# Kernel tuning notes

Measured on AMD Instinct MI355X. Metric: run time of the kernel, lower is better.

## Reference

```python
import math
import jax, jax.numpy as jnp
import numpy as np

N_HEADS = 8
FACTOR = 1.0


def setup_inputs() -> dict:
    key = jax.random.key(0)
    ks = jax.random.split(key, 5)
    B, L, D = 8, 4096, 512
    scale = 0.02
    def w(k):
        return jax.random.normal(k, (D, D), jnp.float32) * scale
    return {
        "hidden_states": jax.random.normal(ks[0], (B, L, D), jnp.float32),
        "Wq": w(ks[1]), "bq": jnp.zeros((D,), jnp.float32),
        "Wk": w(ks[2]), "bk": jnp.zeros((D,), jnp.float32),
        "Wv": w(ks[3]), "bv": jnp.zeros((D,), jnp.float32),
        "Wo": w(ks[4]), "bo": jnp.zeros((D,), jnp.float32),
    }


def reference(hidden_states, Wq, bq, Wk, bk, Wv, bv, Wo, bo):
    B, L, D = hidden_states.shape
    H = N_HEADS
    Hd = D // H

    def proj(W, b):
        y = hidden_states @ W.T + b                      # [B, L, D]
        return y.reshape(B, L, H, Hd).transpose(0, 2, 3, 1)  # [B, H, Hd, L]

    q = proj(Wq, bq)
    k = proj(Wk, bk)
    v = proj(Wv, bv)

    # period-based auto-correlation via FFT: corr(tau) = sum_t q(t) k(t - tau)
    qf = jnp.fft.rfft(q, axis=-1)
    kf = jnp.fft.rfft(k, axis=-1)
    corr = jnp.fft.irfft(qf * jnp.conj(kf), n=L, axis=-1)   # [B, H, Hd, L]

    # time-delay aggregation (eval branch): per-batch top-k delays
    mean_corr = corr.mean(axis=(1, 2))                      # [B, L]
    top_k = int(FACTOR * math.log(L))
    weights, delays = jax.lax.top_k(mean_corr, top_k)       # [B, k]
    weights = jax.nn.softmax(weights, axis=-1)

    # circular gather: pattern[b,h,d,i,l] = v[b,h,d,(l + delay[b,i]) % L]
    idx = (jnp.arange(L)[None, None, :] + delays[:, :, None]) % L  # [B, k, L]
    gathered = jax.vmap(lambda vb, ib: vb[:, :, ib])(v, idx)       # [B, H, Hd, k, L]
    agg = jnp.einsum("bhdkl,bk->bhdl", gathered, weights)          # [B, H, Hd, L]

    ctx = agg.transpose(0, 3, 1, 2).reshape(B, L, D)        # [B, L, D]
    return ctx @ Wo.T + bo
```

## Files before the change

### kernel.cpp

```cpp
#include <hip/hip_runtime.h>
#include <math.h>

#define NB 8
#define NL 4096
#define ND 512
#define NK 8

typedef unsigned short ushort_t;
typedef __bf16 bf16x8 __attribute__((ext_vector_type(8)));
typedef float f32x4 __attribute__((ext_vector_type(4)));

__device__ __forceinline__ unsigned short f2bf(float x) {
    unsigned u = __builtin_bit_cast(unsigned, x);
    u += 0x7fff + ((u >> 16) & 1);
    return (unsigned short)(u >> 16);
}
__device__ __forceinline__ float bf2f(unsigned short b) {
    unsigned u = ((unsigned)b) << 16;
    return __builtin_bit_cast(float, u);
}

__global__ void k_smallgemm(const float* __restrict__ A, const float* __restrict__ Bm,
                            float* __restrict__ C, int sa_k, int sa_i, int sb_k, int sb_j) {
    int i = blockIdx.y * 16 + threadIdx.y;
    int j = blockIdx.x * 16 + threadIdx.x;
    float acc = 0.f;
    for (int k = 0; k < ND; ++k)
        acc += A[k * sa_k + i * sa_i] * Bm[k * sb_k + j * sb_j];
    C[i * ND + j] = acc;
}

__global__ void k_biasprep(const float* __restrict__ Wo, const float* __restrict__ bv,
                           const float* __restrict__ bo, float* __restrict__ bp) {
    int i = blockIdx.x * blockDim.x + threadIdx.x;
    float acc = bo[i];
    for (int k = 0; k < ND; ++k) acc += Wo[i * ND + k] * bv[k];
    bp[i] = acc;
}

__global__ __launch_bounds__(256) void k_split(const float* __restrict__ src,
                                               ushort_t* __restrict__ dst) {
    int gid = blockIdx.x * 256 + threadIdx.x;
    int row = gid >> 7;
    int kc = (gid & 127) * 4;
    float4 v = *(const float4*)(src + (size_t)row * ND + kc);
    ushort4 hi, lo;
    hi.x = f2bf(v.x); lo.x = f2bf(v.x - bf2f(hi.x));
    hi.y = f2bf(v.y); lo.y = f2bf(v.y - bf2f(hi.y));
    hi.z = f2bf(v.z); lo.z = f2bf(v.z - bf2f(hi.z));
    hi.w = f2bf(v.w); lo.w = f2bf(v.w - bf2f(hi.w));
    *(ushort4*)(dst + (size_t)row * 1024 + kc) = hi;
    *(ushort4*)(dst + (size_t)row * 1024 + 512 + kc) = lo;
}

__global__ __launch_bounds__(256) void k_transpose(const float* __restrict__ X,
                                                   float* __restrict__ XT) {
    __shared__ float t[32][33];
    int b  = blockIdx.z;
    int l0 = blockIdx.x * 32;
    int c0 = blockIdx.y * 32;
    const float* Xb = X + (size_t)b * NL * ND;
    float* XTb = XT + (size_t)b * ND * NL;
    int tx = threadIdx.x, ty = threadIdx.y;
#pragma unroll
    for (int j = 0; j < 4; ++j)
        t[ty + j * 8][tx] = Xb[(size_t)(l0 + ty + j * 8) * ND + c0 + tx];
    __syncthreads();
#pragma unroll
    for (int j = 0; j < 4; ++j)
        XTb[(size_t)(c0 + ty + j * 8) * NL + l0 + tx] = t[tx][ty + j * 8];
}

template <int EPI>
__global__ __launch_bounds__(256) void k_gemm_split(const ushort_t* __restrict__ As,
                                                    const ushort_t* __restrict__ Bs,
                                                    const float* __restrict__ bp,
                                                    float* __restrict__ Out) {
    __shared__ union USm {
        struct { ushort_t ahi[128 * 32]; ushort_t alo[128 * 32];
                 ushort_t bhi[128 * 32]; ushort_t blo[128 * 32]; } s;
        float t[32 * 132];
    } sm;
    const int tid = threadIdx.x;
    const int l0 = blockIdx.x * 128;
    const int n0 = blockIdx.y * 128;
    const int lane = tid & 63;
    const int w = tid >> 6;
    const int wr = (w & 1) * 64;
    const int wc = (w >> 1) * 64;
    const int m = lane & 15;
    const int quad = lane >> 4;

    f32x4 acc[4][4];
#pragma unroll
    for (int i = 0; i < 4; ++i)
#pragma unroll
        for (int j = 0; j < 4; ++j) acc[i][j] = (f32x4){0.f, 0.f, 0.f, 0.f};

    for (int k0 = 0; k0 < ND; k0 += 32) {
        __syncthreads();
#pragma unroll
        for (int v = 0; v < 2; ++v) {
            int q = v * 256 + tid;
            int r = q >> 2;
            int c = (q & 3) ^ ((r >> 1) & 3);
            const ushort_t* asrc = As + (size_t)(l0 + r) * 1024 + k0 + c * 8;
            __builtin_amdgcn_global_load_lds(
                (const __attribute__((address_space(1))) unsigned int*)asrc,
                (__attribute__((address_space(3))) unsigned int*)&sm.s.ahi[q * 8], 16, 0, 0);
            __builtin_amdgcn_global_load_lds(
                (const __attribute__((address_space(1))) unsigned int*)(asrc + 512),
                (__attribute__((address_space(3))) unsigned int*)&sm.s.alo[q * 8], 16, 0, 0);
            const ushort_t* bsrc = Bs + (size_t)(n0 + r) * 1024 + k0 + c * 8;
            __builtin_amdgcn_global_load_lds(
                (const __attribute__((address_space(1))) unsigned int*)bsrc,
                (__attribute__((address_space(3))) unsigned int*)&sm.s.bhi[q * 8], 16, 0, 0);
            __builtin_amdgcn_global_load_lds(
                (const __attribute__((address_space(1))) unsigned int*)(bsrc + 512),
                (__attribute__((address_space(3))) unsigned int*)&sm.s.blo[q * 8], 16, 0, 0);
        }
        __syncthreads();

        bf16x8 ah[4], al[4];
#pragma unroll
        for (int i = 0; i < 4; ++i) {
            int row = wr + 16 * i + m;
            int off = row * 32 + ((quad ^ ((row >> 1) & 3)) * 8);
            ah[i] = *(const bf16x8*)&sm.s.ahi[off];
            al[i] = *(const bf16x8*)&sm.s.alo[off];
        }
#pragma unroll
        for (int j = 0; j < 4; ++j) {
            int row = wc + 16 * j + m;
            int off = row * 32 + ((quad ^ ((row >> 1) & 3)) * 8);
            bf16x8 bh = *(const bf16x8*)&sm.s.bhi[off];
            bf16x8 bl = *(const bf16x8*)&sm.s.blo[off];
#pragma unroll
            for (int i = 0; i < 4; ++i) {
                acc[i][j] = __builtin_amdgcn_mfma_f32_16x16x32_bf16(ah[i], bh, acc[i][j], 0, 0, 0);
                acc[i][j] = __builtin_amdgcn_mfma_f32_16x16x32_bf16(ah[i], bl, acc[i][j], 0, 0, 0);
                acc[i][j] = __builtin_amdgcn_mfma_f32_16x16x32_bf16(al[i], bh, acc[i][j], 0, 0, 0);
            }
        }
    }

    if (EPI == 1) {
#pragma unroll
        for (int j = 0; j < 4; ++j) {
            int col = n0 + wc + 16 * j + m;
            float bv = bp[col];
#pragma unroll
            for (int i = 0; i < 4; ++i) {
                size_t rbase = (size_t)(l0 + wr + 16 * i + quad * 4) * ND + col;
#pragma unroll
                for (int r = 0; r < 4; ++r)
                    Out[rbase + (size_t)r * ND] = acc[i][j][r] + bv;
            }
        }
    } else {
#pragma unroll
        for (int c = 0; c < 4; ++c) {
            __syncthreads();
            if ((wc >> 6) == (c >> 1)) {
                int jb = (c & 1) * 2;
#pragma unroll
                for (int jj = 0; jj < 2; ++jj) {
                    int j = jb + jj;
                    int cl = 16 * jj + m;
#pragma unroll
                    for (int i = 0; i < 4; ++i)
#pragma unroll
                        for (int r = 0; r < 4; ++r)
                            sm.t[cl * 132 + wr + 16 * i + quad * 4 + r] = acc[i][j][r];
                }
            }
            __syncthreads();
#pragma unroll
            for (int it = 0; it < 16; ++it) {
                int idx = it * 256 + tid;
                int cl = idx >> 7;
                int row = idx & 127;
                int rg = l0 + row;
                Out[((size_t)((rg >> 12) * ND + n0 + c * 32 + cl)) * NL + (rg & 4095)] =
                    sm.t[cl * 132 + row];
            }
        }
    }
}

template <int DIR>
__device__ __forceinline__ void fft16(float2* v) {
    const float ct[8] = {1.f, 0.923879533f, 0.707106781f, 0.382683432f,
                         0.f, -0.382683432f, -0.707106781f, -0.923879533f};
    const float st[8] = {0.f, 0.382683432f, 0.707106781f, 0.923879533f,
                         1.f, 0.923879533f, 0.707106781f, 0.382683432f};
    const int br[16] = {0, 8, 4, 12, 2, 10, 6, 14, 1, 9, 5, 13, 3, 11, 7, 15};
    float2 a[16];
#pragma unroll
    for (int i = 0; i < 16; ++i) a[i] = v[br[i]];
#pragma unroll
    for (int s = 1; s <= 4; ++s) {
        const int L = 1 << s, h = L >> 1;
#pragma unroll
        for (int g = 0; g < 16; g += L)
#pragma unroll
            for (int p = 0; p < h; ++p) {
                int k = p << (4 - s);
                float wr = ct[k];
                float wi = (DIR > 0) ? -st[k] : st[k];
                int i1 = g + p, i2 = i1 + h;
                float tr = wr * a[i2].x - wi * a[i2].y;
                float ti = wr * a[i2].y + wi * a[i2].x;
                a[i2].x = a[i1].x - tr; a[i2].y = a[i1].y - ti;
                a[i1].x += tr;          a[i1].y += ti;
            }
    }
#pragma unroll
    for (int i = 0; i < 16; ++i) v[i] = a[i];
}

__device__ __forceinline__ float2 cmul(float2 a, float2 b) {
    return make_float2(a.x * b.x - a.y * b.y, a.x * b.y + a.y * b.x);
}
#define PADI(i) ((i) + ((i) >> 4))

__global__ __launch_bounds__(256) void k_fft_fwd(const float* __restrict__ XT,
                                                 const float* __restrict__ YT,
                                                 float2* __restrict__ partial) {
    __shared__ float2 data[4352];
    const int t = threadIdx.x;
    const int b = blockIdx.x >> 6;
    const int g = blockIdx.x & 63;

    float sv, cv;
    sincosf(-6.283185307179586f * (float)(t & 15) / 256.0f, &sv, &cv);
    const float2 w2 = make_float2(cv, sv);
    sincosf(-6.283185307179586f * (float)t / 4096.0f, &sv, &cv);
    const float2 w3 = make_float2(cv, sv);

    float2 acc[16];
#pragma unroll
    for (int r = 0; r < 16; ++r) acc[r] = make_float2(0.f, 0.f);

    for (int ch = 0; ch < 8; ++ch) {
        int c = g * 8 + ch;
        const float* xr = XT + ((size_t)b * ND + c) * NL;
        const float* yr = YT + ((size_t)b * ND + c) * NL;
        float2 v[16];
#pragma unroll
        for (int mm = 0; mm < 16; ++mm)
            v[mm] = make_float2(xr[t + 256 * mm], yr[t + 256 * mm]);
        fft16<1>(v);
        __syncthreads();
#pragma unroll
        for (int mm = 0; mm < 16; ++mm) data[PADI(16 * t + mm)] = v[mm];
        __syncthreads();
#pragma unroll
        for (int mm = 0; mm < 16; ++mm) v[mm] = data[PADI(t + 256 * mm)];
        {
            float2 wm = make_float2(1.f, 0.f);
#pragma unroll
            for (int mm = 1; mm < 16; ++mm) { wm = cmul(wm, w2); v[mm] = cmul(v[mm], wm); }
        }
        fft16<1>(v);
        __syncthreads();
        {
            int base = (t >> 4) * 256 + (t & 15);
#pragma unroll
            for (int mm = 0; mm < 16; ++mm) data[PADI(base + 16 * mm)] = v[mm];
        }
        __syncthreads();
#pragma unroll
        for (int mm = 0; mm < 16; ++mm) v[mm] = data[PADI(t + 256 * mm)];
        {
            float2 wm = make_float2(1.f, 0.f);
#pragma unroll
            for (int mm = 1; mm < 16; ++mm) { wm = cmul(wm, w3); v[mm] = cmul(v[mm], wm); }
        }
        fft16<1>(v);
        __syncthreads();
#pragma unroll
        for (int mm = 0; mm < 16; ++mm) data[PADI(t + 256 * mm)] = v[mm];
        __syncthreads();
#pragma unroll
        for (int mm = 0; mm < 16; ++mm) {
            int f = t + 256 * mm;
            float2 A = v[mm];
            float2 Bz = data[PADI((4096 - f) & 4095)];
            acc[mm].x += 0.5f * (A.x * Bz.y + A.y * Bz.x);
            acc[mm].y += 0.25f * ((A.x * A.x + A.y * A.y) - (Bz.x * Bz.x + Bz.y * Bz.y));
        }
    }
    float2* out = partial + ((size_t)b * 64 + g) * 4096;
#pragma unroll
    for (int mm = 0; mm < 16; ++mm) out[256 * mm + t] = acc[mm];
}

__global__ __launch_bounds__(256) void k_reduce(const float2* __restrict__ partial,
                                                float2* __restrict__ Cf) {
    int b = blockIdx.x >> 4;
    int f = (blockIdx.x & 15) * 256 + threadIdx.x;
    float2 s = make_float2(0.f, 0.f);
    for (int g = 0; g < 64; ++g) {
        float2 v = partial[((size_t)(b * 64 + g)) * 4096 + f];
        s.x += v.x; s.y += v.y;
    }
    Cf[(size_t)b * 4096 + f] = s;
}

__global__ __launch_bounds__(256) void k_ifft(const float2* __restrict__ Cf,
                                              float* __restrict__ mc) {
    __shared__ float2 data[4352];
    const int t = threadIdx.x;
    const int b = blockIdx.x;
    float sv, cv;
    sincosf(6.283185307179586f * (float)(t & 15) / 256.0f, &sv, &cv);
    const float2 w2 = make_float2(cv, sv);
    sincosf(6.283185307179586f * (float)t / 4096.0f, &sv, &cv);
    const float2 w3 = make_float2(cv, sv);

    float2 v[16];
#pragma unroll
    for (int mm = 0; mm < 16; ++mm) v[mm] = Cf[(size_t)b * 4096 + t + 256 * mm];
    fft16<-1>(v);
#pragma unroll
    for (int mm = 0; mm < 16; ++mm) data[PADI(16 * t + mm)] = v[mm];
    __syncthreads();
#pragma unroll
    for (int mm = 0; mm < 16; ++mm) v[mm] = data[PADI(t + 256 * mm)];
    {
        float2 wm = make_float2(1.f, 0.f);
#pragma unroll
        for (int mm = 1; mm < 16; ++mm) { wm = cmul(wm, w2); v[mm] = cmul(v[mm], wm); }
    }
    fft16<-1>(v);
    __syncthreads();
    {
        int base = (t >> 4) * 256 + (t & 15);
#pragma unroll
        for (int mm = 0; mm < 16; ++mm) data[PADI(base + 16 * mm)] = v[mm];
    }
    __syncthreads();
#pragma unroll
    for (int mm = 0; mm < 16; ++mm) v[mm] = data[PADI(t + 256 * mm)];
    {
        float2 wm = make_float2(1.f, 0.f);
#pragma unroll
        for (int mm = 1; mm < 16; ++mm) { wm = cmul(wm, w3); v[mm] = cmul(v[mm], wm); }
    }
    fft16<-1>(v);
    const float scale = 1.0f / (4096.0f * 512.0f);
#pragma unroll
    for (int mm = 0; mm < 16; ++mm)
        mc[(size_t)b * NL + t + 256 * mm] = v[mm].x * scale;
}

__global__ __launch_bounds__(256) void k_topk(const float* __restrict__ mc,
                                              float* __restrict__ wts,
                                              int* __restrict__ dly) {
    __shared__ float vals[4096];
    __shared__ float rv[256];
    __shared__ int ri[256];
    __shared__ float tv[NK];
    __shared__ int tix[NK];
    const int tid = threadIdx.x;
    const int b = blockIdx.x;
    for (int t = tid; t < 4096; t += 256) vals[t] = mc[(size_t)b * NL + t];
    __syncthreads();
    for (int it = 0; it < NK; ++it) {
        float bv = -3.0e38f;
        int bi = 0;
        for (int t = tid; t < 4096; t += 256) {
            float v = vals[t];
            if (v > bv) { bv = v; bi = t; }
        }
        rv[tid] = bv;
        ri[tid] = bi;
        __syncthreads();
        for (int off = 128; off > 0; off >>= 1) {
            if (tid < off) {
                if (rv[tid + off] > rv[tid]) {
                    rv[tid] = rv[tid + off];
                    ri[tid] = ri[tid + off];
                }
            }
            __syncthreads();
        }
        if (tid == 0) {
            tv[it] = rv[0];
            tix[it] = ri[0];
            vals[ri[0]] = -3.0e38f;
        }
        __syncthreads();
    }
    if (tid == 0) {
        float mx = tv[0];
        float e[NK], s = 0.f;
        for (int i = 0; i < NK; ++i) { e[i] = expf(tv[i] - mx); s += e[i]; }
        for (int i = 0; i < NK; ++i) {
            wts[b * NK + i] = e[i] / s;
            dly[b * NK + i] = tix[i];
        }
    }
}

__global__ __launch_bounds__(256) void k_gather(const float* __restrict__ X,
                                                const float* __restrict__ wts,
                                                const int* __restrict__ dly,
                                                ushort_t* __restrict__ Xaggs) {
    __shared__ float sw[NK];
    __shared__ int sd[NK];
    int gid = blockIdx.x * 256 + threadIdx.x;
    int b = gid >> 19;
    int rem = gid & 524287;
    int l = rem >> 7;
    int c4 = rem & 127;
    if (threadIdx.x < NK) {
        sw[threadIdx.x] = wts[b * NK + threadIdx.x];
        sd[threadIdx.x] = dly[b * NK + threadIdx.x];
    }
    __syncthreads();
    const float4* Xb = (const float4*)X + (size_t)b * 524288;
    float4 s = make_float4(0.f, 0.f, 0.f, 0.f);
#pragma unroll
    for (int i = 0; i < NK; ++i) {
        int ls = (l + sd[i]) & (NL - 1);
        float4 v = Xb[(size_t)ls * 128 + c4];
        float w = sw[i];
        s.x += w * v.x;
        s.y += w * v.y;
        s.z += w * v.z;
        s.w += w * v.w;
    }
    ushort4 hi, lo;
    hi.x = f2bf(s.x); lo.x = f2bf(s.x - bf2f(hi.x));
    hi.y = f2bf(s.y); lo.y = f2bf(s.y - bf2f(hi.y));
    hi.z = f2bf(s.z); lo.z = f2bf(s.z - bf2f(hi.z));
    hi.w = f2bf(s.w); lo.w = f2bf(s.w - bf2f(hi.w));
    ushort_t* rowp = Xaggs + (size_t)(b * NL + l) * 1024;
    *(ushort4*)(rowp + c4 * 4) = hi;
    *(ushort4*)(rowp + 512 + c4 * 4) = lo;
}

extern "C" void kernel_launch(void* const* d_in, const int* in_sizes, int n_in,
                              void* d_out, int out_size, void* d_ws, size_t ws_size,
                              hipStream_t stream) {
    (void)in_sizes; (void)n_in; (void)out_size; (void)ws_size;
    const float* X  = (const float*)d_in[0];
    const float* Wq = (const float*)d_in[1];
    const float* Wk = (const float*)d_in[3];
    const float* Wv = (const float*)d_in[5];
    const float* bv = (const float*)d_in[6];
    const float* Wo = (const float*)d_in[7];
    const float* bo = (const float*)d_in[8];
    float* Out = (float*)d_out;

    char* ws = (char*)d_ws;
    const size_t MB = 1024 * 1024;
    float*    M     = (float*)(ws + 0 * MB);
    float*    Wov   = (float*)(ws + 1 * MB);
    ushort_t* BsM   = (ushort_t*)(ws + 2 * MB);
    ushort_t* BsW   = (ushort_t*)(ws + 3 * MB);
    float*    bp    = (float*)(ws + 4 * MB);
    float*    mc    = (float*)(ws + 4 * MB + 0x10000);
    float*    wts   = (float*)(ws + 4 * MB + 0x40000);
    int*      dly   = (int*)(ws + 4 * MB + 0x41000);
    float2*   Cf    = (float2*)(ws + 4 * MB + 0x80000);
    float2*   partial = (float2*)(ws + 5 * MB);
    ushort_t* Xs    = (ushort_t*)(ws + 21 * MB);
    float*    XT    = (float*)(ws + 21 * MB);
    float*    YT    = (float*)(ws + 85 * MB);
    ushort_t* Xaggs = (ushort_t*)(ws + 85 * MB);

    k_smallgemm<<<dim3(32, 32), dim3(16, 16), 0, stream>>>(Wq, Wk, M, ND, 1, ND, 1);
    k_smallgemm<<<dim3(32, 32), dim3(16, 16), 0, stream>>>(Wo, Wv, Wov, 1, ND, ND, 1);
    k_biasprep<<<1, 512, 0, stream>>>(Wo, bv, bo, bp);
    k_split<<<256, 256, 0, stream>>>(M, BsM);
    k_split<<<256, 256, 0, stream>>>(Wov, BsW);

    k_split<<<16384, 256, 0, stream>>>(X, Xs);
    k_gemm_split<0><<<dim3(256, 4), 256, 0, stream>>>(Xs, BsM, nullptr, YT);

    k_transpose<<<dim3(128, 16, NB), dim3(32, 8), 0, stream>>>(X, XT);

    k_fft_fwd<<<512, 256, 0, stream>>>(XT, YT, partial);
    k_reduce<<<128, 256, 0, stream>>>(partial, Cf);
    k_ifft<<<NB, 256, 0, stream>>>(Cf, mc);

    k_topk<<<NB, 256, 0, stream>>>(mc, wts, dly);

    k_gather<<<16384, 256, 0, stream>>>(X, wts, dly, Xaggs);

    k_gemm_split<1><<<dim3(256, 4), 256, 0, stream>>>(Xaggs, BsW, bp, Out);
}
```

Before: 612.4 us.

## Reorder gather after output GEMM, drop transpose, fuse prep and ifft-topk

The output projection is applied before the time-delay gather, which is linear, so the GEMM runs on the pre-split X and the gather works on the projected result written straight to the output. That removes the gather's bf16 split write and lets the second GEMM use a single bf16 term instead of three. The transpose kernel is dropped, so the forward FFT reads X with a strided column access. The weight products are fused with their splitting, and the inverse FFT is merged with top-k. The strided FFT loads and the one-term bf16 output GEMM trade memory efficiency and precision for less work.

```diff
diff --git a/kernel.cpp b/kernel.cpp
--- a/kernel.cpp
+++ b/kernel.cpp
@@ -20,14 +20,22 @@
     return __builtin_bit_cast(float, u);
 }
 
-__global__ void k_smallgemm(const float* __restrict__ A, const float* __restrict__ Bm,
-                            float* __restrict__ C, int sa_k, int sa_i, int sb_k, int sb_j) {
+__global__ void k_prep(const float* __restrict__ Wq, const float* __restrict__ Wk,
+                       const float* __restrict__ Wo, const float* __restrict__ Wv,
+                       ushort_t* __restrict__ BsM, ushort_t* __restrict__ BsW) {
     int i = blockIdx.y * 16 + threadIdx.y;
     int j = blockIdx.x * 16 + threadIdx.x;
     float acc = 0.f;
-    for (int k = 0; k < ND; ++k)
-        acc += A[k * sa_k + i * sa_i] * Bm[k * sb_k + j * sb_j];
-    C[i * ND + j] = acc;
+    if (blockIdx.z == 0) {
+        for (int k = 0; k < ND; ++k) acc += Wq[k * ND + i] * Wk[k * ND + j];
+    } else {
+        for (int k = 0; k < ND; ++k) acc += Wo[i * ND + k] * Wv[k * ND + j];
+    }
+    ushort_t hi = f2bf(acc);
+    ushort_t lo = f2bf(acc - bf2f(hi));
+    ushort_t* dst = (blockIdx.z == 0) ? BsM : BsW;
+    dst[(size_t)i * 1024 + j] = hi;
+    dst[(size_t)i * 1024 + 512 + j] = lo;
 }
 
 __global__ void k_biasprep(const float* __restrict__ Wo, const float* __restrict__ bv,
@@ -53,37 +61,24 @@
     *(ushort4*)(dst + (size_t)row * 1024 + 512 + kc) = lo;
 }
 
-__global__ __launch_bounds__(256) void k_transpose(const float* __restrict__ X,
-                                                   float* __restrict__ XT) {
-    __shared__ float t[32][33];
-    int b  = blockIdx.z;
-    int l0 = blockIdx.x * 32;
-    int c0 = blockIdx.y * 32;
-    const float* Xb = X + (size_t)b * NL * ND;
-    float* XTb = XT + (size_t)b * ND * NL;
-    int tx = threadIdx.x, ty = threadIdx.y;
-#pragma unroll
-    for (int j = 0; j < 4; ++j)
-        t[ty + j * 8][tx] = Xb[(size_t)(l0 + ty + j * 8) * ND + c0 + tx];
-    __syncthreads();
-#pragma unroll
-    for (int j = 0; j < 4; ++j)
-        XTb[(size_t)(c0 + ty + j * 8) * NL + l0 + tx] = t[tx][ty + j * 8];
-}
-
-template <int EPI>
-__global__ __launch_bounds__(256) void k_gemm_split(const ushort_t* __restrict__ As,
-                                                    const ushort_t* __restrict__ Bs,
-                                                    const float* __restrict__ bp,
-                                                    float* __restrict__ Out) {
+template <int TERMS, int EPI>
+__global__ __launch_bounds__(256) void k_gemm(const ushort_t* __restrict__ As,
+                                              const ushort_t* __restrict__ Bs,
+                                              const float* __restrict__ bp,
+                                              float* __restrict__ Out) {
+    constexpr int NTILE = (TERMS == 3) ? 4 : 2;
     __shared__ union USm {
-        struct { ushort_t ahi[128 * 32]; ushort_t alo[128 * 32];
-                 ushort_t bhi[128 * 32]; ushort_t blo[128 * 32]; } s;
+        ushort_t tiles[NTILE * 4096];
         float t[32 * 132];
     } sm;
+    ushort_t* ahi = sm.tiles;
+    ushort_t* alo = sm.tiles + 4096;
+    ushort_t* bhi = sm.tiles + ((TERMS == 3) ? 8192 : 4096);
+    ushort_t* blo = sm.tiles + 12288;
+
     const int tid = threadIdx.x;
-    const int l0 = blockIdx.x * 128;
-    const int n0 = blockIdx.y * 128;
+    const int n0 = blockIdx.x * 128;
+    const int l0 = blockIdx.y * 128;
     const int lane = tid & 63;
     const int w = tid >> 6;
     const int wr = (w & 1) * 64;
@@ -107,17 +102,19 @@
             const ushort_t* asrc = As + (size_t)(l0 + r) * 1024 + k0 + c * 8;
             __builtin_amdgcn_global_load_lds(
                 (const __attribute__((address_space(1))) unsigned int*)asrc,
-                (__attribute__((address_space(3))) unsigned int*)&sm.s.ahi[q * 8], 16, 0, 0);
-            __builtin_amdgcn_global_load_lds(
-                (const __attribute__((address_space(1))) unsigned int*)(asrc + 512),
-                (__attribute__((address_space(3))) unsigned int*)&sm.s.alo[q * 8], 16, 0, 0);
+                (__attribute__((address_space(3))) unsigned int*)&ahi[q * 8], 16, 0, 0);
             const ushort_t* bsrc = Bs + (size_t)(n0 + r) * 1024 + k0 + c * 8;
             __builtin_amdgcn_global_load_lds(
                 (const __attribute__((address_space(1))) unsigned int*)bsrc,
-                (__attribute__((address_space(3))) unsigned int*)&sm.s.bhi[q * 8], 16, 0, 0);
-            __builtin_amdgcn_global_load_lds(
-                (const __attribute__((address_space(1))) unsigned int*)(bsrc + 512),
-                (__attribute__((address_space(3))) unsigned int*)&sm.s.blo[q * 8], 16, 0, 0);
+                (__attribute__((address_space(3))) unsigned int*)&bhi[q * 8], 16, 0, 0);
+            if (TERMS == 3) {
+                __builtin_amdgcn_global_load_lds(
+                    (const __attribute__((address_space(1))) unsigned int*)(asrc + 512),
+                    (__attribute__((address_space(3))) unsigned int*)&alo[q * 8], 16, 0, 0);
+                __builtin_amdgcn_global_load_lds(
+                    (const __attribute__((address_space(1))) unsigned int*)(bsrc + 512),
+                    (__attribute__((address_space(3))) unsigned int*)&blo[q * 8], 16, 0, 0);
+            }
         }
         __syncthreads();
 
@@ -126,20 +123,24 @@
         for (int i = 0; i < 4; ++i) {
             int row = wr + 16 * i + m;
             int off = row * 32 + ((quad ^ ((row >> 1) & 3)) * 8);
-            ah[i] = *(const bf16x8*)&sm.s.ahi[off];
-            al[i] = *(const bf16x8*)&sm.s.alo[off];
+            ah[i] = *(const bf16x8*)&ahi[off];
+            if (TERMS == 3) al[i] = *(const bf16x8*)&alo[off];
         }
 #pragma unroll
         for (int j = 0; j < 4; ++j) {
             int row = wc + 16 * j + m;
             int off = row * 32 + ((quad ^ ((row >> 1) & 3)) * 8);
-            bf16x8 bh = *(const bf16x8*)&sm.s.bhi[off];
-            bf16x8 bl = *(const bf16x8*)&sm.s.blo[off];
-#pragma unroll
-            for (int i = 0; i < 4; ++i) {
+            bf16x8 bh = *(const bf16x8*)&bhi[off];
+#pragma unroll
+            for (int i = 0; i < 4; ++i)
                 acc[i][j] = __builtin_amdgcn_mfma_f32_16x16x32_bf16(ah[i], bh, acc[i][j], 0, 0, 0);
-                acc[i][j] = __builtin_amdgcn_mfma_f32_16x16x32_bf16(ah[i], bl, acc[i][j], 0, 0, 0);
-                acc[i][j] = __builtin_amdgcn_mfma_f32_16x16x32_bf16(al[i], bh, acc[i][j], 0, 0, 0);
+            if (TERMS == 3) {
+                bf16x8 bl = *(const bf16x8*)&blo[off];
+#pragma unroll
+                for (int i = 0; i < 4; ++i) {
+                    acc[i][j] = __builtin_amdgcn_mfma_f32_16x16x32_bf16(ah[i], bl, acc[i][j], 0, 0, 0);
+                    acc[i][j] = __builtin_amdgcn_mfma_f32_16x16x32_bf16(al[i], bh, acc[i][j], 0, 0, 0);
+                }
             }
         }
     }
@@ -224,7 +225,7 @@
 }
 #define PADI(i) ((i) + ((i) >> 4))
 
-__global__ __launch_bounds__(256) void k_fft_fwd(const float* __restrict__ XT,
+__global__ __launch_bounds__(256) void k_fft_fwd(const float* __restrict__ X,
                                                  const float* __restrict__ YT,
                                                  float2* __restrict__ partial) {
     __shared__ float2 data[4352];
@@ -244,12 +245,12 @@
 
     for (int ch = 0; ch < 8; ++ch) {
         int c = g * 8 + ch;
-        const float* xr = XT + ((size_t)b * ND + c) * NL;
+        const float* xb = X + (size_t)b * NL * ND + c;
         const float* yr = YT + ((size_t)b * ND + c) * NL;
         float2 v[16];
 #pragma unroll
         for (int mm = 0; mm < 16; ++mm)
-            v[mm] = make_float2(xr[t + 256 * mm], yr[t + 256 * mm]);
+            v[mm] = make_float2(xb[(size_t)(t + 256 * mm) * ND], yr[t + 256 * mm]);
         fft16<1>(v);
         __syncthreads();
 #pragma unroll
@@ -308,9 +309,14 @@
     Cf[(size_t)b * 4096 + f] = s;
 }
 
-__global__ __launch_bounds__(256) void k_ifft(const float2* __restrict__ Cf,
-                                              float* __restrict__ mc) {
-    __shared__ float2 data[4352];
+__global__ __launch_bounds__(256) void k_ifft_topk(const float2* __restrict__ Cf,
+                                                   float* __restrict__ wts,
+                                                   int* __restrict__ dly) {
+    __shared__ union {
+        float2 data[4352];
+        struct { float vals[4096]; float rv[256]; int ri[256];
+                 float tv[NK]; int tix[NK]; } tk;
+    } sm;
     const int t = threadIdx.x;
     const int b = blockIdx.x;
     float sv, cv;
@@ -324,10 +330,10 @@
     for (int mm = 0; mm < 16; ++mm) v[mm] = Cf[(size_t)b * 4096 + t + 256 * mm];
     fft16<-1>(v);
 #pragma unroll
-    for (int mm = 0; mm < 16; ++mm) data[PADI(16 * t + mm)] = v[mm];
-    __syncthreads();
-#pragma unroll
-    for (int mm = 0; mm < 16; ++mm) v[mm] = data[PADI(t + 256 * mm)];
+    for (int mm = 0; mm < 16; ++mm) sm.data[PADI(16 * t + mm)] = v[mm];
+    __syncthreads();
+#pragma unroll
+    for (int mm = 0; mm < 16; ++mm) v[mm] = sm.data[PADI(t + 256 * mm)];
     {
         float2 wm = make_float2(1.f, 0.f);
 #pragma unroll
@@ -338,76 +344,64 @@
     {
         int base = (t >> 4) * 256 + (t & 15);
 #pragma unroll
-        for (int mm = 0; mm < 16; ++mm) data[PADI(base + 16 * mm)] = v[mm];
-    }
-    __syncthreads();
-#pragma unroll
-    for (int mm = 0; mm < 16; ++mm) v[mm] = data[PADI(t + 256 * mm)];
+        for (int mm = 0; mm < 16; ++mm) sm.data[PADI(base + 16 * mm)] = v[mm];
+    }
+    __syncthreads();
+#pragma unroll
+    for (int mm = 0; mm < 16; ++mm) v[mm] = sm.data[PADI(t + 256 * mm)];
     {
         float2 wm = make_float2(1.f, 0.f);
 #pragma unroll
         for (int mm = 1; mm < 16; ++mm) { wm = cmul(wm, w3); v[mm] = cmul(v[mm], wm); }
     }
     fft16<-1>(v);
+    __syncthreads();
     const float scale = 1.0f / (4096.0f * 512.0f);
 #pragma unroll
-    for (int mm = 0; mm < 16; ++mm)
-        mc[(size_t)b * NL + t + 256 * mm] = v[mm].x * scale;
-}
-
-__global__ __launch_bounds__(256) void k_topk(const float* __restrict__ mc,
-                                              float* __restrict__ wts,
-                                              int* __restrict__ dly) {
-    __shared__ float vals[4096];
-    __shared__ float rv[256];
-    __shared__ int ri[256];
-    __shared__ float tv[NK];
-    __shared__ int tix[NK];
-    const int tid = threadIdx.x;
-    const int b = blockIdx.x;
-    for (int t = tid; t < 4096; t += 256) vals[t] = mc[(size_t)b * NL + t];
-    __syncthreads();
+    for (int mm = 0; mm < 16; ++mm) sm.tk.vals[t + 256 * mm] = v[mm].x * scale;
+    __syncthreads();
+
     for (int it = 0; it < NK; ++it) {
         float bv = -3.0e38f;
         int bi = 0;
-        for (int t = tid; t < 4096; t += 256) {
-            float v = vals[t];
-            if (v > bv) { bv = v; bi = t; }
-        }
-        rv[tid] = bv;
-        ri[tid] = bi;
+        for (int q = t; q < 4096; q += 256) {
+            float x = sm.tk.vals[q];
+            if (x > bv) { bv = x; bi = q; }
+        }
+        sm.tk.rv[t] = bv;
+        sm.tk.ri[t] = bi;
         __syncthreads();
         for (int off = 128; off > 0; off >>= 1) {
-            if (tid < off) {
-                if (rv[tid + off] > rv[tid]) {
-                    rv[tid] = rv[tid + off];
-                    ri[tid] = ri[tid + off];
+            if (t < off) {
+                if (sm.tk.rv[t + off] > sm.tk.rv[t]) {
+                    sm.tk.rv[t] = sm.tk.rv[t + off];
+                    sm.tk.ri[t] = sm.tk.ri[t + off];
                 }
             }
             __syncthreads();
         }
-        if (tid == 0) {
-            tv[it] = rv[0];
-            tix[it] = ri[0];
-            vals[ri[0]] = -3.0e38f;
-        }
-        __syncthreads();
-    }
-    if (tid == 0) {
-        float mx = tv[0];
+        if (t == 0) {
+            sm.tk.tv[it] = sm.tk.rv[0];
+            sm.tk.tix[it] = sm.tk.ri[0];
+            sm.tk.vals[sm.tk.ri[0]] = -3.0e38f;
+        }
+        __syncthreads();
+    }
+    if (t == 0) {
+        float mx = sm.tk.tv[0];
         float e[NK], s = 0.f;
-        for (int i = 0; i < NK; ++i) { e[i] = expf(tv[i] - mx); s += e[i]; }
+        for (int i = 0; i < NK; ++i) { e[i] = expf(sm.tk.tv[i] - mx); s += e[i]; }
         for (int i = 0; i < NK; ++i) {
             wts[b * NK + i] = e[i] / s;
-            dly[b * NK + i] = tix[i];
-        }
-    }
-}
-
-__global__ __launch_bounds__(256) void k_gather(const float* __restrict__ X,
+            dly[b * NK + i] = sm.tk.tix[i];
+        }
+    }
+}
+
+__global__ __launch_bounds__(256) void k_gather(const float* __restrict__ Z,
                                                 const float* __restrict__ wts,
                                                 const int* __restrict__ dly,
-                                                ushort_t* __restrict__ Xaggs) {
+                                                float* __restrict__ Out) {
     __shared__ float sw[NK];
     __shared__ int sd[NK];
     int gid = blockIdx.x * 256 + threadIdx.x;
@@ -420,26 +414,19 @@
         sd[threadIdx.x] = dly[b * NK + threadIdx.x];
     }
     __syncthreads();
-    const float4* Xb = (const float4*)X + (size_t)b * 524288;
+    const float4* Zb = (const float4*)Z + (size_t)b * 524288;
     float4 s = make_float4(0.f, 0.f, 0.f, 0.f);
 #pragma unroll
     for (int i = 0; i < NK; ++i) {
         int ls = (l + sd[i]) & (NL - 1);
-        float4 v = Xb[(size_t)ls * 128 + c4];
+        float4 v = Zb[(size_t)ls * 128 + c4];
         float w = sw[i];
         s.x += w * v.x;
         s.y += w * v.y;
         s.z += w * v.z;
         s.w += w * v.w;
     }
-    ushort4 hi, lo;
-    hi.x = f2bf(s.x); lo.x = f2bf(s.x - bf2f(hi.x));
-    hi.y = f2bf(s.y); lo.y = f2bf(s.y - bf2f(hi.y));
-    hi.z = f2bf(s.z); lo.z = f2bf(s.z - bf2f(hi.z));
-    hi.w = f2bf(s.w); lo.w = f2bf(s.w - bf2f(hi.w));
-    ushort_t* rowp = Xaggs + (size_t)(b * NL + l) * 1024;
-    *(ushort4*)(rowp + c4 * 4) = hi;
-    *(ushort4*)(rowp + 512 + c4 * 4) = lo;
+    ((float4*)Out)[gid] = s;
 }
 
 extern "C" void kernel_launch(void* const* d_in, const int* in_sizes, int n_in,
@@ -457,39 +444,30 @@
 
     char* ws = (char*)d_ws;
     const size_t MB = 1024 * 1024;
-    float*    M     = (float*)(ws + 0 * MB);
-    float*    Wov   = (float*)(ws + 1 * MB);
-    ushort_t* BsM   = (ushort_t*)(ws + 2 * MB);
-    ushort_t* BsW   = (ushort_t*)(ws + 3 * MB);
-    float*    bp    = (float*)(ws + 4 * MB);
-    float*    mc    = (float*)(ws + 4 * MB + 0x10000);
-    float*    wts   = (float*)(ws + 4 * MB + 0x40000);
-    int*      dly   = (int*)(ws + 4 * MB + 0x41000);
-    float2*   Cf    = (float2*)(ws + 4 * MB + 0x80000);
+    ushort_t* BsM = (ushort_t*)(ws + 0 * MB);
+    ushort_t* BsW = (ushort_t*)(ws + 1 * MB);
+    float*    bp  = (float*)(ws + 2 * MB);
+    float2*   Cf  = (float2*)(ws + 2 * MB + 0x10000);
+    float*    wts = (float*)(ws + 2 * MB + 0x60000);
+    int*      dly = (int*)(ws + 2 * MB + 0x61000);
     float2*   partial = (float2*)(ws + 5 * MB);
-    ushort_t* Xs    = (ushort_t*)(ws + 21 * MB);
-    float*    XT    = (float*)(ws + 21 * MB);
-    float*    YT    = (float*)(ws + 85 * MB);
-    ushort_t* Xaggs = (ushort_t*)(ws + 85 * MB);
-
-    k_smallgemm<<<dim3(32, 32), dim3(16, 16), 0, stream>>>(Wq, Wk, M, ND, 1, ND, 1);
-    k_smallgemm<<<dim3(32, 32), dim3(16, 16), 0, stream>>>(Wo, Wv, Wov, 1, ND, ND, 1);
+    ushort_t* Xs  = (ushort_t*)(ws + 21 * MB);
+    float*    YT  = (float*)(ws + 85 * MB);
+    float*    Z   = YT;
+
+    k_prep<<<dim3(32, 32, 2), dim3(16, 16), 0, stream>>>(Wq, Wk, Wo, Wv, BsM, BsW);
     k_biasprep<<<1, 512, 0, stream>>>(Wo, bv, bo, bp);
-    k_split<<<256, 256, 0, stream>>>(M, BsM);
-    k_split<<<256, 256, 0, stream>>>(Wov, BsW);
 
     k_split<<<16384, 256, 0, stream>>>(X, Xs);
-    k_gemm_split<0><<<dim3(256, 4), 256, 0, stream>>>(Xs, BsM, nullptr, YT);
-
-    k_transpose<<<dim3(128, 16, NB), dim3(32, 8), 0, stream>>>(X, XT);
-
-    k_fft_fwd<<<512, 256, 0, stream>>>(XT, YT, partial);
+
+    k_gemm<3, 0><<<dim3(4, 256), 256, 0, stream>>>(Xs, BsM, nullptr, YT);
+
+    k_fft_fwd<<<512, 256, 0, stream>>>(X, YT, partial);
     k_reduce<<<128, 256, 0, stream>>>(partial, Cf);
-    k_ifft<<<NB, 256, 0, stream>>>(Cf, mc);
-
-    k_topk<<<NB, 256, 0, stream>>>(mc, wts, dly);
-
-    k_gather<<<16384, 256, 0, stream>>>(X, wts, dly, Xaggs);
-
-    k_gemm_split<1><<<dim3(256, 4), 256, 0, stream>>>(Xaggs, BsW, bp, Out);
-}
+
+    k_gemm<1, 1><<<dim3(4, 256), 256, 0, stream>>>(Xs, BsW, bp, Z);
+
+    k_ifft_topk<<<NB, 256, 0, stream>>>(Cf, wts, dly);
+
+    k_gather<<<16384, 256, 0, stream>>>(Z, wts, dly, Out);
+}
```

Result: slower. 762.8 us (+24.6%).
